# Kernel tuning notes

Hardware: AMD Instinct MI355X
Metric: run time of the kernel (lower is better)

The kernel has to match this reference:

```python
import jax, jax.numpy as jnp
import numpy as np

B, S, D, H = 2, 2048, 1024, 16
DK = D // H


def setup_inputs() -> dict:
    key = jax.random.key(0)
    ks = jax.random.split(key, 8)
    Q = jax.random.normal(ks[0], (B, S, D), dtype=jnp.float32)
    K = jax.random.normal(ks[1], (B, S, D), dtype=jnp.float32)
    V = jax.random.normal(ks[2], (B, S, D), dtype=jnp.float32)
    scale = 0.02
    W_q = jax.random.normal(ks[3], (D, D), dtype=jnp.float32) * scale
    W_k = jax.random.normal(ks[4], (D, D), dtype=jnp.float32) * scale
    W_v = jax.random.normal(ks[5], (D, D), dtype=jnp.float32) * scale
    W_o = jax.random.normal(ks[6], (D, D), dtype=jnp.float32) * scale
    b_q = jnp.zeros((D,), jnp.float32)
    b_k = jnp.zeros((D,), jnp.float32)
    b_v = jnp.zeros((D,), jnp.float32)
    b_o = jnp.zeros((D,), jnp.float32)
    # causal mask, broadcastable [1,1,S,S]; mask==0 positions are masked out
    mask = jnp.tril(jnp.ones((S, S), jnp.int32))[None, None, :, :]
    return dict(Q=Q, K=K, V=V, W_q=W_q, b_q=b_q, W_k=W_k, b_k=b_k,
                W_v=W_v, b_v=b_v, W_o=W_o, b_o=b_o, mask=mask)


def reference(Q, K, V, W_q, b_q, W_k, b_k, W_v, b_v, W_o, b_o, mask):
    # linear projections (torch Linear equivalent up to weight layout)
    q = Q @ W_q + b_q   # [B,S,D]
    k = K @ W_k + b_k
    v = V @ W_v + b_v
    # split heads -> [B,H,S,DK]
    q = q.reshape(B, S, H, DK).transpose(0, 2, 1, 3)
    k = k.reshape(B, S, H, DK).transpose(0, 2, 1, 3)
    v = v.reshape(B, S, H, DK).transpose(0, 2, 1, 3)
    # scaled dot-product attention with explicit [B,H,S,S] scores
    scores = jnp.einsum('bhqd,bhkd->bhqk', q, k) / jnp.sqrt(jnp.float32(DK))
    scores = jnp.where(mask == 0, jnp.float32(-1e9), scores)
    attn = jax.nn.softmax(scores, axis=-1)
    out = jnp.einsum('bhqk,bhkd->bhqd', attn, v)
    # merge heads and output projection
    out = out.transpose(0, 2, 1, 3).reshape(B, S, D)
    return out @ W_o + b_o
```

## Files before the change

### kernel.cpp

```cpp
#include <hip/hip_runtime.h>


typedef unsigned short u16;
typedef __attribute__((ext_vector_type(8))) short s8v;
typedef __attribute__((ext_vector_type(4))) float f4v;

#define S_ 2048
#define D_ 1024
#define H_ 16
#define DK_ 64

__device__ __forceinline__ u16 f2bf(float f) {
  unsigned u = __builtin_bit_cast(unsigned, f);
  u += 0x7fffu + ((u >> 16) & 1u);
  return (u16)(u >> 16);
}
__device__ __forceinline__ u16 f2bf_t(float f) {
  return (u16)(__builtin_bit_cast(unsigned, f) >> 16);
}

__device__ __forceinline__ void gld_lds16(const u16* g, u16* l) {
  __builtin_amdgcn_global_load_lds(
      (const __attribute__((address_space(1))) unsigned int*)g,
      (__attribute__((address_space(3))) unsigned int*)l, 16, 0, 0);
}

__global__ __launch_bounds__(256) void prep(
    const float* __restrict__ Q, const float* __restrict__ K, const float* __restrict__ V,
    u16* __restrict__ Qc, u16* __restrict__ Kc, u16* __restrict__ Vc,
    const float* __restrict__ W0, const float* __restrict__ W1,
    const float* __restrict__ W2, const float* __restrict__ W3,
    u16* __restrict__ T0, u16* __restrict__ T1, u16* __restrict__ T2, u16* __restrict__ T3) {
  int bid = blockIdx.x, tid = threadIdx.x;
  if (bid < 3072) {
    int z = bid >> 10, t = bid & 1023;
    const float* s = z == 0 ? Q : z == 1 ? K : V;
    u16*         d = z == 0 ? Qc : z == 1 ? Kc : Vc;
    const int n4 = (2 * S_ * D_) / 4;
    for (int idx = t * 256 + tid; idx < n4; idx += 1024 * 256) {
      float4 f = ((const float4*)s)[idx];
      unsigned lo = (unsigned)f2bf(f.x) | ((unsigned)f2bf(f.y) << 16);
      unsigned hi = (unsigned)f2bf(f.z) | ((unsigned)f2bf(f.w) << 16);
      ((uint2*)d)[idx] = make_uint2(lo, hi);
    }
  } else {
    int wb = bid - 3072;
    int z = wb >> 10, t = wb & 1023;
    const float* W = z == 0 ? W0 : z == 1 ? W1 : z == 2 ? W2 : W3;
    u16*         T = z == 0 ? T0 : z == 1 ? T1 : z == 2 ? T2 : T3;
    __shared__ float tile[32][33];
    int tx = tid & 31, ty = tid >> 5;
    int c0 = (t & 31) * 32, r0 = (t >> 5) * 32;
#pragma unroll
    for (int i = 0; i < 32; i += 8)
      tile[ty + i][tx] = W[(size_t)(r0 + ty + i) * D_ + c0 + tx];
    __syncthreads();
#pragma unroll
    for (int i = 0; i < 32; i += 8)
      T[(size_t)(c0 + ty + i) * D_ + r0 + tx] = f2bf(tile[tx][ty + i]);
  }
}

#define BK_ 64

template <int MI, int NJ, int MODE>
__device__ __forceinline__ void gemm_core(const u16* __restrict__ A, const u16* __restrict__ Bt,
                                          const float* __restrict__ bias, void* __restrict__ out,
                                          float oscale, u16* lds) {
  constexpr int BM = MI * 32;
  constexpr int BN = NJ * 32;
  u16* Al = lds;
  u16* Bl = lds + BM * BK_;
  int tid = threadIdx.x;
  int w = tid >> 6, lane = tid & 63, quad = lane >> 4, col = lane & 15;
  int wm = (w >> 1) * (MI * 16), wn = (w & 1) * (NJ * 16);
  int m0 = blockIdx.y * BM, n0 = blockIdx.x * BN;
  f4v acc[MI][NJ] = {};
  const u16* Ag = A + (size_t)m0 * 1024;
  const u16* Bg = Bt + (size_t)n0 * 1024;
  int sr = tid >> 3, ss = tid & 7;

  for (int k0 = 0; k0 < 1024; k0 += BK_) {
    __syncthreads();
#pragma unroll
    for (int c = 0; c < BM / 32; ++c) {
      int r = c * 32 + sr;
      int gs = ss ^ (r & 7);
      gld_lds16(Ag + (size_t)r * 1024 + k0 + gs * 8, &Al[r * BK_ + ss * 8]);
    }
#pragma unroll
    for (int c = 0; c < BN / 32; ++c) {
      int r = c * 32 + sr;
      int gs = ss ^ (r & 7);
      gld_lds16(Bg + (size_t)r * 1024 + k0 + gs * 8, &Bl[r * BK_ + ss * 8]);
    }
    __syncthreads();
#pragma unroll
    for (int hf = 0; hf < 2; ++hf) {
      s8v af[MI], bfr[NJ];
#pragma unroll
      for (int i = 0; i < MI; ++i) {
        int row = wm + i * 16 + col;
        int sl = (hf * 4 + quad) ^ (row & 7);
        af[i] = *(const s8v*)&Al[row * BK_ + sl * 8];
      }
#pragma unroll
      for (int j = 0; j < NJ; ++j) {
        int row = wn + j * 16 + col;
        int sl = (hf * 4 + quad) ^ (row & 7);
        bfr[j] = *(const s8v*)&Bl[row * BK_ + sl * 8];
      }
#pragma unroll
      for (int i = 0; i < MI; ++i)
#pragma unroll
        for (int j = 0; j < NJ; ++j)
          acc[i][j] = __builtin_amdgcn_mfma_f32_16x16x32_bf16(af[i], bfr[j], acc[i][j], 0, 0, 0);
    }
  }

  if (MODE == 1) {
    __syncthreads();
    u16* scr = lds + w * 2304;
    int h = (n0 + wn) >> 6;
    int dkl = lane & 31, sh = (lane >> 5) * 32;
    int mg0 = m0 + wm + sh;
    int bb = mg0 >> 11, s0g = mg0 & 2047;
    u16* ob = (u16*)out + ((size_t)(bb * H_ + h) * DK_) * S_;
#pragma unroll
    for (int t = 0; t < 2; ++t) {
#pragma unroll
      for (int j2 = 2 * t; j2 < 2 * t + 2; ++j2) {
        float bv = bias[n0 + wn + j2 * 16 + col];
        int rloc = j2 * 16 + col - t * 32;
#pragma unroll
        for (int i = 0; i < MI; ++i)
#pragma unroll
          for (int r = 0; r < 4; ++r)
            scr[rloc * 72 + i * 16 + quad * 4 + r] = f2bf(acc[i][j2][r] + bv);
      }
      __builtin_amdgcn_wave_barrier();
      u16* op = ob + (size_t)(t * 32 + dkl) * S_ + s0g;
#pragma unroll
      for (int c = 0; c < 4; ++c)
        *(uint4*)&op[c * 8] = *(const uint4*)&scr[dkl * 72 + sh + c * 8];
      __builtin_amdgcn_wave_barrier();
    }
    return;
  }

#pragma unroll
  for (int i = 0; i < MI; ++i) {
#pragma unroll
    for (int j = 0; j < NJ; ++j) {
      int n = n0 + wn + j * 16 + col;
      float bb = bias[n];
#pragma unroll
      for (int r = 0; r < 4; ++r) {
        int m = m0 + wm + i * 16 + quad * 4 + r;
        float v = (acc[i][j][r] + bb) * oscale;
        if (MODE == 2) {
          ((float*)out)[(size_t)m * 1024 + n] = v;
        } else {
          int b = m >> 11, s = m & 2047, h = n >> 6, dk = n & 63;
          ((u16*)out)[((size_t)(b * H_ + h) * S_ + s) * DK_ + dk] = f2bf(v);
        }
      }
    }
  }
}

#define CEXPQ 0.18033688f

__global__ __launch_bounds__(256) void gemm_qkv(
    const u16* __restrict__ A0, const u16* __restrict__ A1, const u16* __restrict__ A2,
    const u16* __restrict__ B0, const u16* __restrict__ B1, const u16* __restrict__ B2,
    const float* __restrict__ bi0, const float* __restrict__ bi1, const float* __restrict__ bi2,
    u16* __restrict__ o0, u16* __restrict__ o1, u16* __restrict__ o2) {
  __shared__ __attribute__((aligned(16))) u16 lds[128 * BK_ + 128 * BK_];
  int z = blockIdx.z;
  const u16* A = z == 0 ? A0 : z == 1 ? A1 : A2;
  const u16* Bt = z == 0 ? B0 : z == 1 ? B1 : B2;
  const float* bias = z == 0 ? bi0 : z == 1 ? bi1 : bi2;
  u16* o = z == 0 ? o0 : z == 1 ? o1 : o2;
  if (z == 2)
    gemm_core<4, 4, 1>(A, Bt, bias, o, 1.0f, lds);
  else
    gemm_core<4, 4, 0>(A, Bt, bias, o, z == 0 ? CEXPQ : 1.0f, lds);
}

__global__ __launch_bounds__(256, 4) void gemm_out(const u16* __restrict__ A, const u16* __restrict__ Bt,
                                                   const float* __restrict__ bias, float* __restrict__ out) {
  __shared__ __attribute__((aligned(16))) u16 lds[64 * BK_ + 64 * BK_];
  gemm_core<2, 2, 2>(A, Bt, bias, out, 1.0f, lds);
}

#define KT_ 64
#define PSTR 72

__global__ __launch_bounds__(512, 4) void attn_fused(const u16* __restrict__ qb, const u16* __restrict__ kb,
                                                     const u16* __restrict__ vtb, u16* __restrict__ ao) {
  __shared__ __attribute__((aligned(16))) u16 Kt[KT_ * PSTR];
  __shared__ __attribute__((aligned(16))) u16 Vts[DK_ * PSTR];
  __shared__ __attribute__((aligned(16))) u16 Pl[8][16 * PSTR];
  int bh = blockIdx.y, b = bh >> 4, h = bh & 15;
  int j = blockIdx.x;
  int tid = threadIdx.x, w = tid >> 6, lane = tid & 63, quad = lane >> 4, col = lane & 15;
  int sub = w & 3;
  int base = (w < 4) ? (31 - j) * 64 : j * 64;
  int qmin = base + sub * 16;
  int nk = (32 - j) * 64;

  const u16* Qh = qb + (size_t)bh * S_ * DK_;
  const u16* Kh = kb + (size_t)bh * S_ * DK_;
  const u16* Vh = vtb + (size_t)bh * DK_ * S_;

  s8v qf0 = *(const s8v*)(Qh + (size_t)(qmin + col) * DK_ + quad * 8);
  s8v qf1 = *(const s8v*)(Qh + (size_t)(qmin + col) * DK_ + 32 + quad * 8);

  f4v O[4] = {};
  float ls[4] = {};

  int st = tid & 255;
  bool stK = tid < 256;
  int srow = st >> 2, soff = (st & 3) * 16;
  u16* sl = stK ? &Kt[srow * PSTR + soff] : &Vts[srow * PSTR + soff];
  const u16* g0 = stK ? Kh + (size_t)srow * DK_ + soff : Vh + (size_t)srow * S_ + soff;
  uint4 preA = *(const uint4*)g0;
  uint4 preB = *(const uint4*)(g0 + 8);

  for (int kt = 0; kt < nk; kt += KT_) {
    __syncthreads();
    *(uint4*)sl = preA;
    *(uint4*)(sl + 8) = preB;
    __syncthreads();
    int kn = kt + KT_;
    if (kn < nk) {
      const u16* gn = stK ? Kh + (size_t)(kn + srow) * DK_ + soff
                          : Vh + (size_t)srow * S_ + kn + soff;
      preA = *(const uint4*)gn;
      preB = *(const uint4*)(gn + 8);
    }
    if (kt > qmin + 15) continue;

    f4v sc[4];
#pragma unroll
    for (int ks = 0; ks < 4; ++ks) {
      s8v kf0 = *(const s8v*)&Kt[(ks * 16 + col) * PSTR + quad * 8];
      s8v kf1 = *(const s8v*)&Kt[(ks * 16 + col) * PSTR + 32 + quad * 8];
      f4v t = {0.f, 0.f, 0.f, 0.f};
      t = __builtin_amdgcn_mfma_f32_16x16x32_bf16(qf0, kf0, t, 0, 0, 0);
      t = __builtin_amdgcn_mfma_f32_16x16x32_bf16(qf1, kf1, t, 0, 0, 0);
      sc[ks] = t;
    }

    bool full = (kt + KT_ - 1 <= qmin);
#pragma unroll
    for (int r = 0; r < 4; ++r) {
      float p0, p1, p2, p3;
      if (full) {
        p0 = exp2f(sc[0][r]);
        p1 = exp2f(sc[1][r]);
        p2 = exp2f(sc[2][r]);
        p3 = exp2f(sc[3][r]);
      } else {
        int qr = qmin + quad * 4 + r;
        p0 = (kt + col)      <= qr ? exp2f(sc[0][r]) : 0.f;
        p1 = (kt + 16 + col) <= qr ? exp2f(sc[1][r]) : 0.f;
        p2 = (kt + 32 + col) <= qr ? exp2f(sc[2][r]) : 0.f;
        p3 = (kt + 48 + col) <= qr ? exp2f(sc[3][r]) : 0.f;
      }
      ls[r] += (p0 + p1) + (p2 + p3);
      int row = quad * 4 + r;
      Pl[w][row * PSTR + col]      = f2bf_t(p0);
      Pl[w][row * PSTR + 16 + col] = f2bf_t(p1);
      Pl[w][row * PSTR + 32 + col] = f2bf_t(p2);
      Pl[w][row * PSTR + 48 + col] = f2bf_t(p3);
    }
    __builtin_amdgcn_wave_barrier();

    s8v pa0 = *(const s8v*)&Pl[w][col * PSTR + quad * 8];
    s8v pa1 = *(const s8v*)&Pl[w][col * PSTR + 32 + quad * 8];
#pragma unroll
    for (int d = 0; d < 4; ++d) {
      s8v vf0 = *(const s8v*)&Vts[(d * 16 + col) * PSTR + quad * 8];
      s8v vf1 = *(const s8v*)&Vts[(d * 16 + col) * PSTR + 32 + quad * 8];
      O[d] = __builtin_amdgcn_mfma_f32_16x16x32_bf16(pa0, vf0, O[d], 0, 0, 0);
      O[d] = __builtin_amdgcn_mfma_f32_16x16x32_bf16(pa1, vf1, O[d], 0, 0, 0);
    }
    __builtin_amdgcn_wave_barrier();
  }

#pragma unroll
  for (int r = 0; r < 4; ++r) {
    float l = ls[r];
    l += __shfl_xor(l, 1);
    l += __shfl_xor(l, 2);
    l += __shfl_xor(l, 4);
    l += __shfl_xor(l, 8);
    float inv = 1.0f / l;
    size_t row = (size_t)(b * S_ + qmin + quad * 4 + r);
#pragma unroll
    for (int d = 0; d < 4; ++d)
      ao[row * D_ + h * DK_ + d * 16 + col] = f2bf(O[d][r] * inv);
  }
}

extern "C" void kernel_launch(void* const* d_in, const int* in_sizes, int n_in,
                              void* d_out, int out_size, void* d_ws, size_t ws_size,
                              hipStream_t stream) {
  const float* Q  = (const float*)d_in[0];
  const float* K  = (const float*)d_in[1];
  const float* V  = (const float*)d_in[2];
  const float* Wq = (const float*)d_in[3];
  const float* bq = (const float*)d_in[4];
  const float* Wk = (const float*)d_in[5];
  const float* bk = (const float*)d_in[6];
  const float* Wv = (const float*)d_in[7];
  const float* bv = (const float*)d_in[8];
  const float* Wo = (const float*)d_in[9];
  const float* bo = (const float*)d_in[10];

  char* p = (char*)d_ws;
  const size_t TEN = (size_t)2 * S_ * D_ * 2;
  const size_t WT  = (size_t)D_ * D_ * 2;
  u16* Qc  = (u16*)p; p += TEN;
  u16* Kc  = (u16*)p; p += TEN;
  u16* Vc  = (u16*)p; p += TEN;
  u16* Wqt = (u16*)p; p += WT;
  u16* Wkt = (u16*)p; p += WT;
  u16* Wvt = (u16*)p; p += WT;
  u16* Wot = (u16*)p; p += WT;
  u16* qb  = (u16*)p; p += TEN;
  u16* kbf = (u16*)p; p += TEN;
  u16* vtb = (u16*)p; p += TEN;
  u16* ao  = (u16*)p; p += TEN;

  prep<<<7168, 256, 0, stream>>>(Q, K, V, Qc, Kc, Vc, Wq, Wk, Wv, Wo, Wqt, Wkt, Wvt, Wot);
  gemm_qkv<<<dim3(D_ / 128, 32, 3), 256, 0, stream>>>(Qc, Kc, Vc, Wqt, Wkt, Wvt, bq, bk, bv, qb, kbf, vtb);
  attn_fused<<<dim3(16, 2 * H_), 512, 0, stream>>>(qb, kbf, vtb, ao);
  gemm_out<<<dim3(D_ / 64, 64), 256, 0, stream>>>(ao, Wot, bo, (float*)d_out);
}
```

Baseline: 238.1 us.

## Give each attention wave 32 query rows and halve block size

The attention kernel now uses 4 waves per block instead of 8. Each wave handles 32 query rows as two 16-row subtiles, so every K/V fragment read from LDS feeds twice as many MFMAs. Staging loads per thread double to keep the K/V tile fill the same, and s_setprio is raised around the MFMA sections. This cuts LDS traffic per FLOP, at the cost of more registers per wave and fewer waves per block, which may reduce latency hiding and occupancy.

```diff
diff --git a/kernel.cpp b/kernel.cpp
--- a/kernel.cpp
+++ b/kernel.cpp
@@ -197,111 +197,137 @@
 #define KT_ 64
 #define PSTR 72
 
-__global__ __launch_bounds__(512, 4) void attn_fused(const u16* __restrict__ qb, const u16* __restrict__ kb,
+__global__ __launch_bounds__(256, 2) void attn_fused(const u16* __restrict__ qb, const u16* __restrict__ kb,
                                                      const u16* __restrict__ vtb, u16* __restrict__ ao) {
   __shared__ __attribute__((aligned(16))) u16 Kt[KT_ * PSTR];
   __shared__ __attribute__((aligned(16))) u16 Vts[DK_ * PSTR];
-  __shared__ __attribute__((aligned(16))) u16 Pl[8][16 * PSTR];
+  __shared__ __attribute__((aligned(16))) u16 Pl[4][32 * PSTR];
   int bh = blockIdx.y, b = bh >> 4, h = bh & 15;
   int j = blockIdx.x;
   int tid = threadIdx.x, w = tid >> 6, lane = tid & 63, quad = lane >> 4, col = lane & 15;
-  int sub = w & 3;
-  int base = (w < 4) ? (31 - j) * 64 : j * 64;
-  int qmin = base + sub * 16;
+  int sub = w & 1;
+  int base = (w < 2) ? (31 - j) * 64 : j * 64;
+  int qmin = base + sub * 32;
   int nk = (32 - j) * 64;
 
   const u16* Qh = qb + (size_t)bh * S_ * DK_;
   const u16* Kh = kb + (size_t)bh * S_ * DK_;
   const u16* Vh = vtb + (size_t)bh * DK_ * S_;
 
-  s8v qf0 = *(const s8v*)(Qh + (size_t)(qmin + col) * DK_ + quad * 8);
-  s8v qf1 = *(const s8v*)(Qh + (size_t)(qmin + col) * DK_ + 32 + quad * 8);
-
-  f4v O[4] = {};
-  float ls[4] = {};
-
-  int st = tid & 255;
-  bool stK = tid < 256;
-  int srow = st >> 2, soff = (st & 3) * 16;
+  s8v qfA[2], qfB[2];
+#pragma unroll
+  for (int s = 0; s < 2; ++s) {
+    qfA[s] = *(const s8v*)(Qh + (size_t)(qmin + s * 16 + col) * DK_ + quad * 8);
+    qfB[s] = *(const s8v*)(Qh + (size_t)(qmin + s * 16 + col) * DK_ + 32 + quad * 8);
+  }
+
+  f4v O[2][4] = {};
+  float ls[2][4] = {};
+
+  int st = tid & 127;
+  bool stK = tid < 128;
+  int srow = st >> 1, soff = (st & 1) * 32;
   u16* sl = stK ? &Kt[srow * PSTR + soff] : &Vts[srow * PSTR + soff];
   const u16* g0 = stK ? Kh + (size_t)srow * DK_ + soff : Vh + (size_t)srow * S_ + soff;
-  uint4 preA = *(const uint4*)g0;
-  uint4 preB = *(const uint4*)(g0 + 8);
+  uint4 pre[4];
+#pragma unroll
+  for (int c = 0; c < 4; ++c) pre[c] = *(const uint4*)(g0 + c * 8);
 
   for (int kt = 0; kt < nk; kt += KT_) {
     __syncthreads();
-    *(uint4*)sl = preA;
-    *(uint4*)(sl + 8) = preB;
+#pragma unroll
+    for (int c = 0; c < 4; ++c) *(uint4*)(sl + c * 8) = pre[c];
     __syncthreads();
     int kn = kt + KT_;
     if (kn < nk) {
       const u16* gn = stK ? Kh + (size_t)(kn + srow) * DK_ + soff
                           : Vh + (size_t)srow * S_ + kn + soff;
-      preA = *(const uint4*)gn;
-      preB = *(const uint4*)(gn + 8);
-    }
-    if (kt > qmin + 15) continue;
-
-    f4v sc[4];
+#pragma unroll
+      for (int c = 0; c < 4; ++c) pre[c] = *(const uint4*)(gn + c * 8);
+    }
+    if (kt > qmin + 31) continue;
+
+    f4v sc[2][4];
+    __builtin_amdgcn_s_setprio(1);
 #pragma unroll
     for (int ks = 0; ks < 4; ++ks) {
       s8v kf0 = *(const s8v*)&Kt[(ks * 16 + col) * PSTR + quad * 8];
       s8v kf1 = *(const s8v*)&Kt[(ks * 16 + col) * PSTR + 32 + quad * 8];
-      f4v t = {0.f, 0.f, 0.f, 0.f};
-      t = __builtin_amdgcn_mfma_f32_16x16x32_bf16(qf0, kf0, t, 0, 0, 0);
-      t = __builtin_amdgcn_mfma_f32_16x16x32_bf16(qf1, kf1, t, 0, 0, 0);
-      sc[ks] = t;
-    }
-
-    bool full = (kt + KT_ - 1 <= qmin);
-#pragma unroll
-    for (int r = 0; r < 4; ++r) {
-      float p0, p1, p2, p3;
-      if (full) {
-        p0 = exp2f(sc[0][r]);
-        p1 = exp2f(sc[1][r]);
-        p2 = exp2f(sc[2][r]);
-        p3 = exp2f(sc[3][r]);
-      } else {
-        int qr = qmin + quad * 4 + r;
-        p0 = (kt + col)      <= qr ? exp2f(sc[0][r]) : 0.f;
-        p1 = (kt + 16 + col) <= qr ? exp2f(sc[1][r]) : 0.f;
-        p2 = (kt + 32 + col) <= qr ? exp2f(sc[2][r]) : 0.f;
-        p3 = (kt + 48 + col) <= qr ? exp2f(sc[3][r]) : 0.f;
-      }
-      ls[r] += (p0 + p1) + (p2 + p3);
-      int row = quad * 4 + r;
-      Pl[w][row * PSTR + col]      = f2bf_t(p0);
-      Pl[w][row * PSTR + 16 + col] = f2bf_t(p1);
-      Pl[w][row * PSTR + 32 + col] = f2bf_t(p2);
-      Pl[w][row * PSTR + 48 + col] = f2bf_t(p3);
+#pragma unroll
+      for (int s = 0; s < 2; ++s) {
+        f4v t = {0.f, 0.f, 0.f, 0.f};
+        t = __builtin_amdgcn_mfma_f32_16x16x32_bf16(qfA[s], kf0, t, 0, 0, 0);
+        t = __builtin_amdgcn_mfma_f32_16x16x32_bf16(qfB[s], kf1, t, 0, 0, 0);
+        sc[s][ks] = t;
+      }
+    }
+    __builtin_amdgcn_s_setprio(0);
+
+#pragma unroll
+    for (int s = 0; s < 2; ++s) {
+      int qs = qmin + s * 16;
+      bool full = (kt + KT_ - 1 <= qs);
+#pragma unroll
+      for (int r = 0; r < 4; ++r) {
+        float p0, p1, p2, p3;
+        if (full) {
+          p0 = exp2f(sc[s][0][r]);
+          p1 = exp2f(sc[s][1][r]);
+          p2 = exp2f(sc[s][2][r]);
+          p3 = exp2f(sc[s][3][r]);
+        } else {
+          int qr = qs + quad * 4 + r;
+          p0 = (kt + col)      <= qr ? exp2f(sc[s][0][r]) : 0.f;
+          p1 = (kt + 16 + col) <= qr ? exp2f(sc[s][1][r]) : 0.f;
+          p2 = (kt + 32 + col) <= qr ? exp2f(sc[s][2][r]) : 0.f;
+          p3 = (kt + 48 + col) <= qr ? exp2f(sc[s][3][r]) : 0.f;
+        }
+        ls[s][r] += (p0 + p1) + (p2 + p3);
+        int row = s * 16 + quad * 4 + r;
+        Pl[w][row * PSTR + col]      = f2bf_t(p0);
+        Pl[w][row * PSTR + 16 + col] = f2bf_t(p1);
+        Pl[w][row * PSTR + 32 + col] = f2bf_t(p2);
+        Pl[w][row * PSTR + 48 + col] = f2bf_t(p3);
+      }
     }
     __builtin_amdgcn_wave_barrier();
 
-    s8v pa0 = *(const s8v*)&Pl[w][col * PSTR + quad * 8];
-    s8v pa1 = *(const s8v*)&Pl[w][col * PSTR + 32 + quad * 8];
+    s8v pa0[2], pa1[2];
+#pragma unroll
+    for (int s = 0; s < 2; ++s) {
+      pa0[s] = *(const s8v*)&Pl[w][(s * 16 + col) * PSTR + quad * 8];
+      pa1[s] = *(const s8v*)&Pl[w][(s * 16 + col) * PSTR + 32 + quad * 8];
+    }
+    __builtin_amdgcn_s_setprio(1);
 #pragma unroll
     for (int d = 0; d < 4; ++d) {
       s8v vf0 = *(const s8v*)&Vts[(d * 16 + col) * PSTR + quad * 8];
       s8v vf1 = *(const s8v*)&Vts[(d * 16 + col) * PSTR + 32 + quad * 8];
-      O[d] = __builtin_amdgcn_mfma_f32_16x16x32_bf16(pa0, vf0, O[d], 0, 0, 0);
-      O[d] = __builtin_amdgcn_mfma_f32_16x16x32_bf16(pa1, vf1, O[d], 0, 0, 0);
-    }
+#pragma unroll
+      for (int s = 0; s < 2; ++s) {
+        O[s][d] = __builtin_amdgcn_mfma_f32_16x16x32_bf16(pa0[s], vf0, O[s][d], 0, 0, 0);
+        O[s][d] = __builtin_amdgcn_mfma_f32_16x16x32_bf16(pa1[s], vf1, O[s][d], 0, 0, 0);
+      }
+    }
+    __builtin_amdgcn_s_setprio(0);
     __builtin_amdgcn_wave_barrier();
   }
 
 #pragma unroll
-  for (int r = 0; r < 4; ++r) {
-    float l = ls[r];
-    l += __shfl_xor(l, 1);
-    l += __shfl_xor(l, 2);
-    l += __shfl_xor(l, 4);
-    l += __shfl_xor(l, 8);
-    float inv = 1.0f / l;
-    size_t row = (size_t)(b * S_ + qmin + quad * 4 + r);
-#pragma unroll
-    for (int d = 0; d < 4; ++d)
-      ao[row * D_ + h * DK_ + d * 16 + col] = f2bf(O[d][r] * inv);
+  for (int s = 0; s < 2; ++s) {
+#pragma unroll
+    for (int r = 0; r < 4; ++r) {
+      float l = ls[s][r];
+      l += __shfl_xor(l, 1);
+      l += __shfl_xor(l, 2);
+      l += __shfl_xor(l, 4);
+      l += __shfl_xor(l, 8);
+      float inv = 1.0f / l;
+      size_t row = (size_t)(b * S_ + qmin + s * 16 + quad * 4 + r);
+#pragma unroll
+      for (int d = 0; d < 4; ++d)
+        ao[row * D_ + h * DK_ + d * 16 + col] = f2bf(O[s][d][r] * inv);
+    }
   }
 }
 
@@ -337,6 +363,6 @@
 
   prep<<<7168, 256, 0, stream>>>(Q, K, V, Qc, Kc, Vc, Wq, Wk, Wv, Wo, Wqt, Wkt, Wvt, Wot);
   gemm_qkv<<<dim3(D_ / 128, 32, 3), 256, 0, stream>>>(Qc, Kc, Vc, Wqt, Wkt, Wvt, bq, bk, bv, qb, kbf, vtb);
-  attn_fused<<<dim3(16, 2 * H_), 512, 0, stream>>>(qb, kbf, vtb, ao);
+  attn_fused<<<dim3(16, 2 * H_), 256, 0, stream>>>(qb, kbf, vtb, ao);
   gemm_out<<<dim3(D_ / 64, 64), 256, 0, stream>>>(ao, Wot, bo, (float*)d_out);
 }
```

Measured after the change: 290.4 us. +21.9%, slower.

## Double-buffer K/V tiles in LDS to drop one barrier per iteration

Applied to the files above, without the earlier changes.

The attention kernel now keeps two LDS buffers for the K and V tiles. Each iteration writes the next tile into the alternate buffer while computing on the current one, so one __syncthreads per iteration goes away. It also raises wave priority with s_setprio around the MFMA blocks. The cost is double the K/V LDS footprint, which may limit occupancy, and a deeper prefetch chain held in registers.

```diff
diff --git a/kernel.cpp b/kernel.cpp
--- a/kernel.cpp
+++ b/kernel.cpp
@@ -199,8 +199,8 @@
 
 __global__ __launch_bounds__(512, 4) void attn_fused(const u16* __restrict__ qb, const u16* __restrict__ kb,
                                                      const u16* __restrict__ vtb, u16* __restrict__ ao) {
-  __shared__ __attribute__((aligned(16))) u16 Kt[KT_ * PSTR];
-  __shared__ __attribute__((aligned(16))) u16 Vts[DK_ * PSTR];
+  __shared__ __attribute__((aligned(16))) u16 Kt[2][KT_ * PSTR];
+  __shared__ __attribute__((aligned(16))) u16 Vts[2][DK_ * PSTR];
   __shared__ __attribute__((aligned(16))) u16 Pl[8][16 * PSTR];
   int bh = blockIdx.y, b = bh >> 4, h = bh & 15;
   int j = blockIdx.x;
@@ -223,71 +223,93 @@
   int st = tid & 255;
   bool stK = tid < 256;
   int srow = st >> 2, soff = (st & 3) * 16;
-  u16* sl = stK ? &Kt[srow * PSTR + soff] : &Vts[srow * PSTR + soff];
-  const u16* g0 = stK ? Kh + (size_t)srow * DK_ + soff : Vh + (size_t)srow * S_ + soff;
-  uint4 preA = *(const uint4*)g0;
-  uint4 preB = *(const uint4*)(g0 + 8);
-
+  int slo = srow * PSTR + soff;
+  const u16* gK = Kh + (size_t)srow * DK_ + soff;
+  const u16* gV = Vh + (size_t)srow * S_ + soff;
+
+  uint4 preA, preB;
+  {
+    const u16* g0 = stK ? gK : gV;
+    preA = *(const uint4*)g0;
+    preB = *(const uint4*)(g0 + 8);
+    u16* d = (stK ? &Kt[0][0] : &Vts[0][0]) + slo;
+    *(uint4*)d = preA;
+    *(uint4*)(d + 8) = preB;
+    const u16* g1 = stK ? gK + (size_t)KT_ * DK_ : gV + KT_;
+    preA = *(const uint4*)g1;
+    preB = *(const uint4*)(g1 + 8);
+  }
+
+  int cur = 0;
   for (int kt = 0; kt < nk; kt += KT_) {
     __syncthreads();
-    *(uint4*)sl = preA;
-    *(uint4*)(sl + 8) = preB;
-    __syncthreads();
-    int kn = kt + KT_;
-    if (kn < nk) {
-      const u16* gn = stK ? Kh + (size_t)(kn + srow) * DK_ + soff
-                          : Vh + (size_t)srow * S_ + kn + soff;
-      preA = *(const uint4*)gn;
-      preB = *(const uint4*)(gn + 8);
-    }
-    if (kt > qmin + 15) continue;
-
-    f4v sc[4];
-#pragma unroll
-    for (int ks = 0; ks < 4; ++ks) {
-      s8v kf0 = *(const s8v*)&Kt[(ks * 16 + col) * PSTR + quad * 8];
-      s8v kf1 = *(const s8v*)&Kt[(ks * 16 + col) * PSTR + 32 + quad * 8];
-      f4v t = {0.f, 0.f, 0.f, 0.f};
-      t = __builtin_amdgcn_mfma_f32_16x16x32_bf16(qf0, kf0, t, 0, 0, 0);
-      t = __builtin_amdgcn_mfma_f32_16x16x32_bf16(qf1, kf1, t, 0, 0, 0);
-      sc[ks] = t;
-    }
-
-    bool full = (kt + KT_ - 1 <= qmin);
-#pragma unroll
-    for (int r = 0; r < 4; ++r) {
-      float p0, p1, p2, p3;
-      if (full) {
-        p0 = exp2f(sc[0][r]);
-        p1 = exp2f(sc[1][r]);
-        p2 = exp2f(sc[2][r]);
-        p3 = exp2f(sc[3][r]);
-      } else {
-        int qr = qmin + quad * 4 + r;
-        p0 = (kt + col)      <= qr ? exp2f(sc[0][r]) : 0.f;
-        p1 = (kt + 16 + col) <= qr ? exp2f(sc[1][r]) : 0.f;
-        p2 = (kt + 32 + col) <= qr ? exp2f(sc[2][r]) : 0.f;
-        p3 = (kt + 48 + col) <= qr ? exp2f(sc[3][r]) : 0.f;
-      }
-      ls[r] += (p0 + p1) + (p2 + p3);
-      int row = quad * 4 + r;
-      Pl[w][row * PSTR + col]      = f2bf_t(p0);
-      Pl[w][row * PSTR + 16 + col] = f2bf_t(p1);
-      Pl[w][row * PSTR + 32 + col] = f2bf_t(p2);
-      Pl[w][row * PSTR + 48 + col] = f2bf_t(p3);
-    }
-    __builtin_amdgcn_wave_barrier();
-
-    s8v pa0 = *(const s8v*)&Pl[w][col * PSTR + quad * 8];
-    s8v pa1 = *(const s8v*)&Pl[w][col * PSTR + 32 + quad * 8];
-#pragma unroll
-    for (int d = 0; d < 4; ++d) {
-      s8v vf0 = *(const s8v*)&Vts[(d * 16 + col) * PSTR + quad * 8];
-      s8v vf1 = *(const s8v*)&Vts[(d * 16 + col) * PSTR + 32 + quad * 8];
-      O[d] = __builtin_amdgcn_mfma_f32_16x16x32_bf16(pa0, vf0, O[d], 0, 0, 0);
-      O[d] = __builtin_amdgcn_mfma_f32_16x16x32_bf16(pa1, vf1, O[d], 0, 0, 0);
-    }
-    __builtin_amdgcn_wave_barrier();
+    if (kt + KT_ < nk) {
+      u16* d = (stK ? &Kt[cur ^ 1][0] : &Vts[cur ^ 1][0]) + slo;
+      *(uint4*)d = preA;
+      *(uint4*)(d + 8) = preB;
+      int k2 = kt + 2 * KT_;
+      if (k2 < nk) {
+        const u16* gn = stK ? gK + (size_t)k2 * DK_ : gV + k2;
+        preA = *(const uint4*)gn;
+        preB = *(const uint4*)(gn + 8);
+      }
+    }
+    if (kt <= qmin + 15) {
+      const u16* Kc = &Kt[cur][0];
+      const u16* Vc = &Vts[cur][0];
+
+      f4v sc[4];
+      __builtin_amdgcn_s_setprio(1);
+#pragma unroll
+      for (int ks = 0; ks < 4; ++ks) {
+        s8v kf0 = *(const s8v*)&Kc[(ks * 16 + col) * PSTR + quad * 8];
+        s8v kf1 = *(const s8v*)&Kc[(ks * 16 + col) * PSTR + 32 + quad * 8];
+        f4v t = {0.f, 0.f, 0.f, 0.f};
+        t = __builtin_amdgcn_mfma_f32_16x16x32_bf16(qf0, kf0, t, 0, 0, 0);
+        t = __builtin_amdgcn_mfma_f32_16x16x32_bf16(qf1, kf1, t, 0, 0, 0);
+        sc[ks] = t;
+      }
+      __builtin_amdgcn_s_setprio(0);
+
+      bool full = (kt + KT_ - 1 <= qmin);
+#pragma unroll
+      for (int r = 0; r < 4; ++r) {
+        float p0, p1, p2, p3;
+        if (full) {
+          p0 = exp2f(sc[0][r]);
+          p1 = exp2f(sc[1][r]);
+          p2 = exp2f(sc[2][r]);
+          p3 = exp2f(sc[3][r]);
+        } else {
+          int qr = qmin + quad * 4 + r;
+          p0 = (kt + col)      <= qr ? exp2f(sc[0][r]) : 0.f;
+          p1 = (kt + 16 + col) <= qr ? exp2f(sc[1][r]) : 0.f;
+          p2 = (kt + 32 + col) <= qr ? exp2f(sc[2][r]) : 0.f;
+          p3 = (kt + 48 + col) <= qr ? exp2f(sc[3][r]) : 0.f;
+        }
+        ls[r] += (p0 + p1) + (p2 + p3);
+        int row = quad * 4 + r;
+        Pl[w][row * PSTR + col]      = f2bf_t(p0);
+        Pl[w][row * PSTR + 16 + col] = f2bf_t(p1);
+        Pl[w][row * PSTR + 32 + col] = f2bf_t(p2);
+        Pl[w][row * PSTR + 48 + col] = f2bf_t(p3);
+      }
+      __builtin_amdgcn_wave_barrier();
+
+      s8v pa0 = *(const s8v*)&Pl[w][col * PSTR + quad * 8];
+      s8v pa1 = *(const s8v*)&Pl[w][col * PSTR + 32 + quad * 8];
+      __builtin_amdgcn_s_setprio(1);
+#pragma unroll
+      for (int d = 0; d < 4; ++d) {
+        s8v vf0 = *(const s8v*)&Vc[(d * 16 + col) * PSTR + quad * 8];
+        s8v vf1 = *(const s8v*)&Vc[(d * 16 + col) * PSTR + 32 + quad * 8];
+        O[d] = __builtin_amdgcn_mfma_f32_16x16x32_bf16(pa0, vf0, O[d], 0, 0, 0);
+        O[d] = __builtin_amdgcn_mfma_f32_16x16x32_bf16(pa1, vf1, O[d], 0, 0, 0);
+      }
+      __builtin_amdgcn_s_setprio(0);
+      __builtin_amdgcn_wave_barrier();
+    }
+    cur ^= 1;
   }
 
 #pragma unroll
```

After: 232.5 us. -2.4%, faster.
